# Performance work log

Measured on AMD Instinct MI355X. Metric: run time of the kernel, lower is better.

The kernel has to match this reference:

```python
import jax, jax.numpy as jnp
import numpy as np

D_MODEL = 512
NUM_HEADS = 8
D_HEAD = D_MODEL // NUM_HEADS
B, S = 2, 4096


def setup_inputs() -> dict:
    key = jax.random.key(0)
    ks = jax.random.split(key, 9)
    scale = 1.0 / np.sqrt(D_MODEL)
    x = jax.random.normal(ks[0], (B, S, D_MODEL), dtype=jnp.float32)
    Wq = jax.random.normal(ks[1], (D_MODEL, D_MODEL), dtype=jnp.float32) * scale
    Wk = jax.random.normal(ks[2], (D_MODEL, D_MODEL), dtype=jnp.float32) * scale
    Wv = jax.random.normal(ks[3], (D_MODEL, D_MODEL), dtype=jnp.float32) * scale
    Wo = jax.random.normal(ks[4], (D_MODEL, D_MODEL), dtype=jnp.float32) * scale
    bq = jnp.zeros((D_MODEL,), jnp.float32)
    bk = jnp.zeros((D_MODEL,), jnp.float32)
    bv = jnp.zeros((D_MODEL,), jnp.float32)
    bo = jnp.zeros((D_MODEL,), jnp.float32)
    return {"x": x, "Wq": Wq, "bq": bq, "Wk": Wk, "bk": bk,
            "Wv": Wv, "bv": bv, "Wo": Wo, "bo": bo}


def _split_heads(t):
    # [B, S, D] -> [B, H, S, d_head]
    b, s, _ = t.shape
    return t.reshape(b, s, NUM_HEADS, D_HEAD).transpose(0, 2, 1, 3)


def reference(x, Wq, bq, Wk, bk, Wv, bv, Wo, bo):
    q = _split_heads(x @ Wq + bq)  # [B,H,S,dh]
    k = _split_heads(x @ Wk + bk)
    v = _split_heads(x @ Wv + bv)
    scores = jnp.einsum("bhqd,bhkd->bhqk", q, k) / jnp.sqrt(
        jnp.asarray(D_HEAD, x.dtype))
    attn = jax.nn.softmax(scores, axis=-1)  # dropout is identity at inference
    out = jnp.einsum("bhqk,bhkd->bhqd", attn, v)  # [B,H,S,dh]
    out = out.transpose(0, 2, 1, 3).reshape(x.shape[0], x.shape[1], D_MODEL)
    return out @ Wo + bo
```

## Files before the change

### kernel.cpp

```cpp
#include <hip/hip_runtime.h>
#include <cstddef>

#define NB   2
#define SEQ  4096
#define DM   512
#define NH   8
#define DH   64
#define MTOT 8192
#define KSPLIT 4
#define KSEQ (SEQ / KSPLIT)

#define QSCALE 0.18033688011112042f

typedef __attribute__((ext_vector_type(8))) short short8;
typedef __attribute__((ext_vector_type(4))) float f32x4;

__device__ __forceinline__ ushort f2bf(float f) {
  unsigned u = __builtin_bit_cast(unsigned, f);
  u += 0x7FFFu + ((u >> 16) & 1u);
  return (ushort)(u >> 16);
}
__device__ __forceinline__ float bf2f(ushort b) {
  return __builtin_bit_cast(float, ((unsigned)b) << 16);
}
__device__ __forceinline__ unsigned cvt_pk_bf16(float lo, float hi) {
  unsigned r;
  asm("v_cvt_pk_bf16_f32 %0, %1, %2" : "=v"(r) : "v"(lo), "v"(hi));
  return r;
}
__device__ __forceinline__ float fexp2(float x) {
#if __has_builtin(__builtin_amdgcn_exp2f)
  return __builtin_amdgcn_exp2f(x);
#else
  float r;
  asm("v_exp_f32 %0, %1" : "=v"(r) : "v"(x));
  return r;
#endif
}

__global__ __launch_bounds__(256)
void prep_all_k(const float* __restrict__ x,
                const float* __restrict__ Wq, const float* __restrict__ Wk,
                const float* __restrict__ Wv, const float* __restrict__ Wo,
                ushort* __restrict__ xb,
                ushort* __restrict__ WTq, ushort* __restrict__ WTk,
                ushort* __restrict__ WTv, ushort* __restrict__ WTh,
                ushort* __restrict__ WTl) {
  __shared__ float t[32][33];
  int bid = blockIdx.x;
  if (bid < 2048) {
    const int i = (bid * 256 + threadIdx.x) * 8;
    float4 a = *(const float4*)(x + i);
    float4 b = *(const float4*)(x + i + 4);
    ushort h[8] = {f2bf(a.x), f2bf(a.y), f2bf(a.z), f2bf(a.w),
                   f2bf(b.x), f2bf(b.y), f2bf(b.z), f2bf(b.w)};
    *(uint4*)(xb + i) = *(const uint4*)h;
    return;
  }
  bid -= 2048;
  const int z = bid >> 8;
  const int rr = bid & 255;
  const float* W = (z == 0) ? Wq : (z == 1) ? Wk : (z == 2) ? Wv : Wo;
  ushort* WT = (z == 0) ? WTq : (z == 1) ? WTk : (z == 2) ? WTv : WTh;
  ushort* WTlo = (z == 3) ? WTl : nullptr;
  const int k0 = (rr & 15) * 32, n0 = (rr >> 4) * 32;
  const int tx = threadIdx.x & 31, ty = threadIdx.x >> 5;
#pragma unroll
  for (int i = 0; i < 32; i += 8)
    t[ty + i][tx] = W[(size_t)(k0 + ty + i) * DM + n0 + tx];
  __syncthreads();
#pragma unroll
  for (int i = 0; i < 32; i += 8) {
    float v = t[tx][ty + i];
    ushort h = f2bf(v);
    WT[(size_t)(n0 + ty + i) * DM + k0 + tx] = h;
    if (WTlo) WTlo[(size_t)(n0 + ty + i) * DM + k0 + tx] = f2bf(v - bf2f(h));
  }
}

__global__ __launch_bounds__(256)
void qkv_gemm_k(const ushort* __restrict__ xb,
                const ushort* __restrict__ WTq, const ushort* __restrict__ WTk,
                const ushort* __restrict__ WTv,
                const float* __restrict__ bq, const float* __restrict__ bk,
                const float* __restrict__ bv,
                ushort* __restrict__ Qb, ushort* __restrict__ Kb,
                ushort* __restrict__ Vb) {
  __shared__ ushort smem[17920];
  ushort (*As)[40] = (ushort(*)[40])smem;
  ushort (*Bs)[40] = (ushort(*)[40])(smem + 5120);

  const int z = blockIdx.z;
  const ushort* WT = (z == 0) ? WTq : (z == 1) ? WTk : WTv;
  const float* bias = (z == 0) ? bq : (z == 1) ? bk : bv;
  ushort* outp = (z == 0) ? Qb : (z == 1) ? Kb : Vb;
  const float oscale = (z == 0) ? QSCALE : 1.0f;

  const int tid = threadIdx.x;
  const int w = tid >> 6, l = tid & 63;
  const int g = l >> 4, l15 = l & 15;
  const int wm = w >> 1, wn = w & 1;
  const int m0 = blockIdx.x * 128;
  const int n0 = blockIdx.y * 128;

  const int ar = tid >> 1, ac = (tid & 1) * 16;
  const ushort* Ag = xb + (size_t)(m0 + ar) * DM + ac;
  const ushort* Bg = WT + (size_t)(n0 + ar) * DM + ac;

  uint4 ra0 = *(const uint4*)(Ag);
  uint4 ra1 = *(const uint4*)(Ag + 8);
  uint4 rb0 = *(const uint4*)(Bg);
  uint4 rb1 = *(const uint4*)(Bg + 8);

  float bfn[4];
#pragma unroll
  for (int fn = 0; fn < 4; ++fn)
    bfn[fn] = bias[n0 + wn * 64 + fn * 16 + l15];

  f32x4 acc[4][4];
#pragma unroll
  for (int fm = 0; fm < 4; ++fm)
#pragma unroll
    for (int fn = 0; fn < 4; ++fn) acc[fm][fn] = (f32x4){0.f, 0.f, 0.f, 0.f};

  for (int k0 = 0; k0 < DM; k0 += 32) {
    __syncthreads();
    *(uint4*)&As[ar][ac]     = ra0;
    *(uint4*)&As[ar][ac + 8] = ra1;
    *(uint4*)&Bs[ar][ac]     = rb0;
    *(uint4*)&Bs[ar][ac + 8] = rb1;
    __syncthreads();
    if (k0 + 32 < DM) {
      ra0 = *(const uint4*)(Ag + k0 + 32);
      ra1 = *(const uint4*)(Ag + k0 + 40);
      rb0 = *(const uint4*)(Bg + k0 + 32);
      rb1 = *(const uint4*)(Bg + k0 + 40);
    }
    short8 af[4], bf[4];
#pragma unroll
    for (int fm = 0; fm < 4; ++fm)
      af[fm] = *(const short8*)&As[wm * 64 + fm * 16 + l15][g * 8];
#pragma unroll
    for (int fn = 0; fn < 4; ++fn)
      bf[fn] = *(const short8*)&Bs[wn * 64 + fn * 16 + l15][g * 8];
#pragma unroll
    for (int fm = 0; fm < 4; ++fm)
#pragma unroll
      for (int fn = 0; fn < 4; ++fn)
        acc[fm][fn] = __builtin_amdgcn_mfma_f32_16x16x32_bf16(
            af[fm], bf[fn], acc[fm][fn], 0, 0, 0);
  }

  __syncthreads();
  ushort (*T)[140] = (ushort(*)[140])smem;
  const int b = m0 >> 12, s0 = m0 & (SEQ - 1);
  const int h0 = n0 >> 6;
  if (z != 2) {
#pragma unroll
    for (int fm = 0; fm < 4; ++fm)
#pragma unroll
      for (int fn = 0; fn < 4; ++fn)
#pragma unroll
        for (int r = 0; r < 4; ++r) {
          int ml = wm * 64 + fm * 16 + g * 4 + r;
          int nl = wn * 64 + fn * 16 + l15;
          T[ml][nl] = f2bf((acc[fm][fn][r] + bfn[fn]) * oscale);
        }
    __syncthreads();
#pragma unroll
    for (int it = 0; it < 8; ++it) {
      int ch = tid + 256 * it;
      int hl = ch >> 10;
      int sl = (ch >> 3) & 127;
      int c8 = (ch & 7) * 8;
      *(uint4*)(outp + ((size_t)(b * NH + h0 + hl) * SEQ + s0 + sl) * DH + c8) =
          *(const uint4*)&T[sl][hl * 64 + c8];
    }
  } else {
#pragma unroll
    for (int fm = 0; fm < 4; ++fm)
#pragma unroll
      for (int fn = 0; fn < 4; ++fn)
#pragma unroll
        for (int r = 0; r < 4; ++r) {
          int ml = wm * 64 + fm * 16 + g * 4 + r;
          int nl = wn * 64 + fn * 16 + l15;
          T[nl][ml] = f2bf(acc[fm][fn][r] + bfn[fn]);
        }
    __syncthreads();
#pragma unroll
    for (int it = 0; it < 8; ++it) {
      int ch = tid + 256 * it;
      int row = ch >> 4;
      int cc = (ch & 15) * 8;
      int n = n0 + row;
      int h = n >> 6, d = n & 63;
      *(uint4*)(outp + ((size_t)(b * NH + h) * DH + d) * SEQ + s0 + cc) =
          *(const uint4*)&T[row][cc];
    }
  }
}

__global__ __launch_bounds__(256)
void combine_k(const ushort* __restrict__ Po, const float* __restrict__ Dn,
               ushort* __restrict__ Ahb, ushort* __restrict__ Alb) {
  const size_t o = (size_t)(blockIdx.x * 256 + threadIdx.x) * 8;
  const int m = (int)(o >> 9);
  const int c = (int)(o & 511);
  const int b = m >> 12, s = m & (SEQ - 1);
  const int h = c >> 6, d = c & 63;
  const int bh = b * NH + h;
  const size_t i0 = ((size_t)bh * SEQ + s) * DH + d;
  const size_t zoff = (size_t)(NB * NH) * SEQ * DH;

  float den = 0.f;
  float v[8];
#pragma unroll
  for (int j = 0; j < 8; ++j) v[j] = 0.f;
#pragma unroll
  for (int z = 0; z < KSPLIT; ++z) {
    den += Dn[((size_t)z * (NB * NH) + bh) * SEQ + s];
    uint4 p = *(const uint4*)(Po + (size_t)z * zoff + i0);
    const unsigned* pu = (const unsigned*)&p;
#pragma unroll
    for (int j = 0; j < 4; ++j) {
      v[2 * j]     += __builtin_bit_cast(float, pu[j] << 16);
      v[2 * j + 1] += __builtin_bit_cast(float, pu[j] & 0xFFFF0000u);
    }
  }
  const float inv = __builtin_amdgcn_rcpf(den);
  ushort hh[8], ll[8];
#pragma unroll
  for (int j = 0; j < 8; ++j) {
    float a = v[j] * inv;
    ushort hb = f2bf(a);
    hh[j] = hb;
    ll[j] = f2bf(a - bf2f(hb));
  }
  *(uint4*)(Ahb + o) = *(const uint4*)hh;
  *(uint4*)(Alb + o) = *(const uint4*)ll;
}

__global__ __launch_bounds__(256)
void oproj_gemm_k(const ushort* __restrict__ Ahb, const ushort* __restrict__ Alb,
                  const ushort* __restrict__ WTh, const ushort* __restrict__ WTl,
                  const float* __restrict__ bo, float* __restrict__ out) {
  __shared__ ushort Ah[128][40];
  __shared__ ushort Al[128][40];
  __shared__ ushort Bh[128][40];
  __shared__ ushort Bl[128][40];

  const int tid = threadIdx.x;
  const int w = tid >> 6, l = tid & 63;
  const int g = l >> 4, l15 = l & 15;
  const int wm = w >> 1, wn = w & 1;
  const int m0 = blockIdx.x * 128;
  const int n0 = blockIdx.y * 128;

  const int ar = tid >> 1, ac = (tid & 1) * 16;

  const ushort* Ahg = Ahb + (size_t)(m0 + ar) * DM + ac;
  const ushort* Alg = Alb + (size_t)(m0 + ar) * DM + ac;
  const ushort* Bhg = WTh + (size_t)(n0 + ar) * DM + ac;
  const ushort* Blg = WTl + (size_t)(n0 + ar) * DM + ac;

  uint4 rah0 = *(const uint4*)(Ahg);
  uint4 rah1 = *(const uint4*)(Ahg + 8);
  uint4 ral0 = *(const uint4*)(Alg);
  uint4 ral1 = *(const uint4*)(Alg + 8);
  uint4 rbh0 = *(const uint4*)(Bhg);
  uint4 rbh1 = *(const uint4*)(Bhg + 8);
  uint4 rbl0 = *(const uint4*)(Blg);
  uint4 rbl1 = *(const uint4*)(Blg + 8);

  float bfn[4];
#pragma unroll
  for (int fn = 0; fn < 4; ++fn)
    bfn[fn] = bo[n0 + wn * 64 + fn * 16 + l15];

  f32x4 acc[4][4];
#pragma unroll
  for (int fm = 0; fm < 4; ++fm)
#pragma unroll
    for (int fn = 0; fn < 4; ++fn) acc[fm][fn] = (f32x4){0.f, 0.f, 0.f, 0.f};

  for (int k0 = 0; k0 < DM; k0 += 32) {
    __syncthreads();
    *(uint4*)&Ah[ar][ac]     = rah0;
    *(uint4*)&Ah[ar][ac + 8] = rah1;
    *(uint4*)&Al[ar][ac]     = ral0;
    *(uint4*)&Al[ar][ac + 8] = ral1;
    *(uint4*)&Bh[ar][ac]     = rbh0;
    *(uint4*)&Bh[ar][ac + 8] = rbh1;
    *(uint4*)&Bl[ar][ac]     = rbl0;
    *(uint4*)&Bl[ar][ac + 8] = rbl1;
    __syncthreads();
    if (k0 + 32 < DM) {
      rah0 = *(const uint4*)(Ahg + k0 + 32);
      rah1 = *(const uint4*)(Ahg + k0 + 40);
      ral0 = *(const uint4*)(Alg + k0 + 32);
      ral1 = *(const uint4*)(Alg + k0 + 40);
      rbh0 = *(const uint4*)(Bhg + k0 + 32);
      rbh1 = *(const uint4*)(Bhg + k0 + 40);
      rbl0 = *(const uint4*)(Blg + k0 + 32);
      rbl1 = *(const uint4*)(Blg + k0 + 40);
    }
    short8 ah[4], al[4], bh[4], bl[4];
#pragma unroll
    for (int fm = 0; fm < 4; ++fm) {
      ah[fm] = *(const short8*)&Ah[wm * 64 + fm * 16 + l15][g * 8];
      al[fm] = *(const short8*)&Al[wm * 64 + fm * 16 + l15][g * 8];
    }
#pragma unroll
    for (int fn = 0; fn < 4; ++fn) {
      bh[fn] = *(const short8*)&Bh[wn * 64 + fn * 16 + l15][g * 8];
      bl[fn] = *(const short8*)&Bl[wn * 64 + fn * 16 + l15][g * 8];
    }
#pragma unroll
    for (int fm = 0; fm < 4; ++fm)
#pragma unroll
      for (int fn = 0; fn < 4; ++fn) {
        f32x4 c = acc[fm][fn];
        c = __builtin_amdgcn_mfma_f32_16x16x32_bf16(ah[fm], bh[fn], c, 0, 0, 0);
        c = __builtin_amdgcn_mfma_f32_16x16x32_bf16(ah[fm], bl[fn], c, 0, 0, 0);
        c = __builtin_amdgcn_mfma_f32_16x16x32_bf16(al[fm], bh[fn], c, 0, 0, 0);
        acc[fm][fn] = c;
      }
  }

#pragma unroll
  for (int fm = 0; fm < 4; ++fm)
#pragma unroll
    for (int fn = 0; fn < 4; ++fn)
#pragma unroll
      for (int r = 0; r < 4; ++r) {
        int mm = m0 + wm * 64 + fm * 16 + g * 4 + r;
        int n = n0 + wn * 64 + fn * 16 + l15;
        out[(size_t)mm * DM + n] = acc[fm][fn][r] + bfn[fn];
      }
}

__global__ __launch_bounds__(256, 4)
void attn_mfma_k(const ushort* __restrict__ Q, const ushort* __restrict__ K,
                 const ushort* __restrict__ VT, ushort* __restrict__ Po,
                 float* __restrict__ Dn) {
  __shared__ ushort Ks[64][72];
  __shared__ unsigned Vt[64][36];

  const int tid = threadIdx.x;
  const int w   = tid >> 6;
  const int l   = tid & 63;
  const int g   = l >> 4;
  const int l15 = l & 15;
  const int bh  = blockIdx.y;
  const int z   = blockIdx.z;
  const int q0  = blockIdx.x * 128 + w * 32;
  const int tb  = z * KSEQ;

  short8 qb[2][2];
#pragma unroll
  for (int qh = 0; qh < 2; ++qh) {
    const ushort* Qrow = Q + ((size_t)bh * SEQ + q0 + qh * 16 + l15) * DH;
    qb[qh][0] = *(const short8*)(Qrow + g * 8);
    qb[qh][1] = *(const short8*)(Qrow + 32 + g * 8);
  }

  short8 vones;
#pragma unroll
  for (int i = 0; i < 8; ++i) vones[i] = (short)0x3F80;

  f32x4 acc[2][4];
  f32x4 accl[2];
#pragma unroll
  for (int qh = 0; qh < 2; ++qh) {
    accl[qh] = (f32x4){0.f, 0.f, 0.f, 0.f};
#pragma unroll
    for (int dt = 0; dt < 4; ++dt) acc[qh][dt] = (f32x4){0.f, 0.f, 0.f, 0.f};
  }

  const ushort* Kg = K + (size_t)bh * SEQ * DH;

  const int rho  = tid >> 2;
  const int kcol = (tid & 3) * 16;
  const int sig  = 32 * ((rho >> 5) & 1) + 8 * ((rho >> 2) & 3) +
                   4 * ((rho >> 4) & 1) + (rho & 3);
  const ushort* Kp = Kg + (size_t)(tb + sig) * DH + kcol;

  const int vrow = tid >> 2;
  const int vcb  = (tid & 3) * 8;
  const unsigned* Vrow =
      (const unsigned*)(VT + ((size_t)bh * DH + vrow) * SEQ) + tb / 2 + vcb;

  uint4 kr0 = *(const uint4*)(Kp);
  uint4 kr1 = *(const uint4*)(Kp + 8);
  uint4 vv0 = *(const uint4*)(Vrow);
  uint4 vv1 = *(const uint4*)(Vrow + 4);

  for (int t0 = 0; t0 < KSEQ; t0 += 64) {
    __syncthreads();
    *(uint4*)&Ks[rho][kcol]     = kr0;
    *(uint4*)&Ks[rho][kcol + 8] = kr1;
    *(uint4*)&Vt[vrow][vcb]     = vv0;
    *(uint4*)&Vt[vrow][vcb + 4] = vv1;
    if (t0 + 64 < KSEQ) {
      kr0 = *(const uint4*)(Kp + (size_t)(t0 + 64) * DH);
      kr1 = *(const uint4*)(Kp + (size_t)(t0 + 64) * DH + 8);
      vv0 = *(const uint4*)(Vrow + (t0 + 64) / 2);
      vv1 = *(const uint4*)(Vrow + (t0 + 64) / 2 + 4);
    }
    __syncthreads();

    f32x4 s[2][4];
    __builtin_amdgcn_s_setprio(1);
#pragma unroll
    for (int nf = 0; nf < 4; ++nf) {
      short8 ka0 = *(const short8*)&Ks[nf * 16 + l15][g * 8];
      short8 ka1 = *(const short8*)&Ks[nf * 16 + l15][32 + g * 8];
#pragma unroll
      for (int qh = 0; qh < 2; ++qh) {
        f32x4 c = (f32x4){0.f, 0.f, 0.f, 0.f};
        c = __builtin_amdgcn_mfma_f32_16x16x32_bf16(ka0, qb[qh][0], c, 0, 0, 0);
        c = __builtin_amdgcn_mfma_f32_16x16x32_bf16(ka1, qb[qh][1], c, 0, 0, 0);
        s[qh][nf] = c;
      }
    }
    __builtin_amdgcn_s_setprio(0);

    short8 pa[2][2];
#pragma unroll
    for (int qh = 0; qh < 2; ++qh) {
      float p[4][4];
#pragma unroll
      for (int nf = 0; nf < 4; ++nf)
#pragma unroll
        for (int r = 0; r < 4; ++r) p[nf][r] = fexp2(s[qh][nf][r]);
      uint4 u0, u1;
      u0.x = cvt_pk_bf16(p[0][0], p[0][1]);
      u0.y = cvt_pk_bf16(p[0][2], p[0][3]);
      u0.z = cvt_pk_bf16(p[1][0], p[1][1]);
      u0.w = cvt_pk_bf16(p[1][2], p[1][3]);
      u1.x = cvt_pk_bf16(p[2][0], p[2][1]);
      u1.y = cvt_pk_bf16(p[2][2], p[2][3]);
      u1.z = cvt_pk_bf16(p[3][0], p[3][1]);
      u1.w = cvt_pk_bf16(p[3][2], p[3][3]);
      pa[qh][0] = __builtin_bit_cast(short8, u0);
      pa[qh][1] = __builtin_bit_cast(short8, u1);
    }

    __builtin_amdgcn_s_setprio(1);
#pragma unroll
    for (int dt = 0; dt < 4; ++dt) {
      short8 vb0 = *(const short8*)&Vt[dt * 16 + l15][4 * g];
      short8 vb1 = *(const short8*)&Vt[dt * 16 + l15][16 + 4 * g];
#pragma unroll
      for (int qh = 0; qh < 2; ++qh) {
        acc[qh][dt] = __builtin_amdgcn_mfma_f32_16x16x32_bf16(pa[qh][0], vb0,
                                                              acc[qh][dt], 0, 0, 0);
        acc[qh][dt] = __builtin_amdgcn_mfma_f32_16x16x32_bf16(pa[qh][1], vb1,
                                                              acc[qh][dt], 0, 0, 0);
      }
    }
#pragma unroll
    for (int qh = 0; qh < 2; ++qh) {
      accl[qh] = __builtin_amdgcn_mfma_f32_16x16x32_bf16(pa[qh][0], vones,
                                                         accl[qh], 0, 0, 0);
      accl[qh] = __builtin_amdgcn_mfma_f32_16x16x32_bf16(pa[qh][1], vones,
                                                         accl[qh], 0, 0, 0);
    }
    __builtin_amdgcn_s_setprio(0);
  }

  const int zo = z * (NB * NH) + bh;
#pragma unroll
  for (int qh = 0; qh < 2; ++qh) {
#pragma unroll
    for (int dt = 0; dt < 4; ++dt)
#pragma unroll
      for (int r = 0; r < 4; ++r) {
        int srow = q0 + qh * 16 + g * 4 + r;
        Po[((size_t)zo * SEQ + srow) * DH + dt * 16 + l15] =
            f2bf(acc[qh][dt][r]);
      }
    if (l15 == 0)
#pragma unroll
      for (int r = 0; r < 4; ++r)
        Dn[(size_t)zo * SEQ + q0 + qh * 16 + g * 4 + r] = accl[qh][r];
  }
}

extern "C" void kernel_launch(void* const* d_in, const int* in_sizes, int n_in,
                              void* d_out, int out_size, void* d_ws, size_t ws_size,
                              hipStream_t stream) {
  const float* x  = (const float*)d_in[0];
  const float* Wq = (const float*)d_in[1];
  const float* bq = (const float*)d_in[2];
  const float* Wk = (const float*)d_in[3];
  const float* bk = (const float*)d_in[4];
  const float* Wv = (const float*)d_in[5];
  const float* bv = (const float*)d_in[6];
  const float* Wo = (const float*)d_in[7];
  const float* bo = (const float*)d_in[8];
  float* out = (float*)d_out;

  const size_t per = (size_t)NB * NH * SEQ * DH;
  const size_t wsz = (size_t)DM * DM;
  ushort* xb  = (ushort*)d_ws;
  ushort* WTq = xb + (size_t)MTOT * DM;
  ushort* WTk = WTq + wsz;
  ushort* WTv = WTk + wsz;
  ushort* WTh = WTv + wsz;
  ushort* WTl = WTh + wsz;
  ushort* Qb  = WTl + wsz;
  ushort* Kb  = Qb + per;
  ushort* Vb  = Kb + per;
  ushort* Po  = Vb + per;
  float*  Dn  = (float*)(Po + (size_t)KSPLIT * per);
  ushort* Ahb = xb;
  ushort* Alb = Qb;

  prep_all_k<<<3072, 256, 0, stream>>>(x, Wq, Wk, Wv, Wo, xb,
                                       WTq, WTk, WTv, WTh, WTl);
  qkv_gemm_k<<<dim3(MTOT / 128, DM / 128, 3), 256, 0, stream>>>(
      xb, WTq, WTk, WTv, bq, bk, bv, Qb, Kb, Vb);
  attn_mfma_k<<<dim3(SEQ / 128, NB * NH, KSPLIT), 256, 0, stream>>>(
      Qb, Kb, Vb, Po, Dn);
  combine_k<<<MTOT * DM / (256 * 8), 256, 0, stream>>>(Po, Dn, Ahb, Alb);
  oproj_gemm_k<<<dim3(MTOT / 128, DM / 128), 256, 0, stream>>>(
      Ahb, Alb, WTh, WTl, bo, out);
}
```

Before: 140.8 us.

## Drop split-bf16 output projection and shrink GEMM M-tiles to 64 rows

The output projection previously used hi/lo bf16 splitting of both activations and Wo, with three MFMAs per tile. It now uses a single bf16 pass, which removes the lo-part buffers, their writes in prep and combine, and two thirds of the oproj MFMA work. Separately, both the QKV and output-projection GEMMs move from 128x128 to 64x128 tiles, doubling the block count to improve occupancy and load balance. The cost is lower output accuracy from the plain bf16 matmul, and less data reuse per tile.

```diff
diff --git a/kernel.cpp b/kernel.cpp
--- a/kernel.cpp
+++ b/kernel.cpp
@@ -44,8 +44,7 @@
                 const float* __restrict__ Wv, const float* __restrict__ Wo,
                 ushort* __restrict__ xb,
                 ushort* __restrict__ WTq, ushort* __restrict__ WTk,
-                ushort* __restrict__ WTv, ushort* __restrict__ WTh,
-                ushort* __restrict__ WTl) {
+                ushort* __restrict__ WTv, ushort* __restrict__ WTh) {
   __shared__ float t[32][33];
   int bid = blockIdx.x;
   if (bid < 2048) {
@@ -62,7 +61,6 @@
   const int rr = bid & 255;
   const float* W = (z == 0) ? Wq : (z == 1) ? Wk : (z == 2) ? Wv : Wo;
   ushort* WT = (z == 0) ? WTq : (z == 1) ? WTk : (z == 2) ? WTv : WTh;
-  ushort* WTlo = (z == 3) ? WTl : nullptr;
   const int k0 = (rr & 15) * 32, n0 = (rr >> 4) * 32;
   const int tx = threadIdx.x & 31, ty = threadIdx.x >> 5;
 #pragma unroll
@@ -70,12 +68,8 @@
     t[ty + i][tx] = W[(size_t)(k0 + ty + i) * DM + n0 + tx];
   __syncthreads();
 #pragma unroll
-  for (int i = 0; i < 32; i += 8) {
-    float v = t[tx][ty + i];
-    ushort h = f2bf(v);
-    WT[(size_t)(n0 + ty + i) * DM + k0 + tx] = h;
-    if (WTlo) WTlo[(size_t)(n0 + ty + i) * DM + k0 + tx] = f2bf(v - bf2f(h));
-  }
+  for (int i = 0; i < 32; i += 8)
+    WT[(size_t)(n0 + ty + i) * DM + k0 + tx] = f2bf(t[tx][ty + i]);
 }
 
 __global__ __launch_bounds__(256)
@@ -86,9 +80,9 @@
                 const float* __restrict__ bv,
                 ushort* __restrict__ Qb, ushort* __restrict__ Kb,
                 ushort* __restrict__ Vb) {
-  __shared__ ushort smem[17920];
+  __shared__ ushort smem[9216];
   ushort (*As)[40] = (ushort(*)[40])smem;
-  ushort (*Bs)[40] = (ushort(*)[40])(smem + 5120);
+  ushort (*Bs)[40] = (ushort(*)[40])(smem + 2560);
 
   const int z = blockIdx.z;
   const ushort* WT = (z == 0) ? WTq : (z == 1) ? WTk : WTv;
@@ -100,15 +94,15 @@
   const int w = tid >> 6, l = tid & 63;
   const int g = l >> 4, l15 = l & 15;
   const int wm = w >> 1, wn = w & 1;
-  const int m0 = blockIdx.x * 128;
+  const int m0 = blockIdx.x * 64;
   const int n0 = blockIdx.y * 128;
 
-  const int ar = tid >> 1, ac = (tid & 1) * 16;
-  const ushort* Ag = xb + (size_t)(m0 + ar) * DM + ac;
-  const ushort* Bg = WT + (size_t)(n0 + ar) * DM + ac;
+  const int arA = tid >> 2, acA = (tid & 3) * 8;
+  const int arB = tid >> 1, acB = (tid & 1) * 16;
+  const ushort* Ag = xb + (size_t)(m0 + arA) * DM + acA;
+  const ushort* Bg = WT + (size_t)(n0 + arB) * DM + acB;
 
   uint4 ra0 = *(const uint4*)(Ag);
-  uint4 ra1 = *(const uint4*)(Ag + 8);
   uint4 rb0 = *(const uint4*)(Bg);
   uint4 rb1 = *(const uint4*)(Bg + 8);
 
@@ -117,34 +111,32 @@
   for (int fn = 0; fn < 4; ++fn)
     bfn[fn] = bias[n0 + wn * 64 + fn * 16 + l15];
 
-  f32x4 acc[4][4];
-#pragma unroll
-  for (int fm = 0; fm < 4; ++fm)
+  f32x4 acc[2][4];
+#pragma unroll
+  for (int fm = 0; fm < 2; ++fm)
 #pragma unroll
     for (int fn = 0; fn < 4; ++fn) acc[fm][fn] = (f32x4){0.f, 0.f, 0.f, 0.f};
 
   for (int k0 = 0; k0 < DM; k0 += 32) {
     __syncthreads();
-    *(uint4*)&As[ar][ac]     = ra0;
-    *(uint4*)&As[ar][ac + 8] = ra1;
-    *(uint4*)&Bs[ar][ac]     = rb0;
-    *(uint4*)&Bs[ar][ac + 8] = rb1;
+    *(uint4*)&As[arA][acA]     = ra0;
+    *(uint4*)&Bs[arB][acB]     = rb0;
+    *(uint4*)&Bs[arB][acB + 8] = rb1;
     __syncthreads();
     if (k0 + 32 < DM) {
       ra0 = *(const uint4*)(Ag + k0 + 32);
-      ra1 = *(const uint4*)(Ag + k0 + 40);
       rb0 = *(const uint4*)(Bg + k0 + 32);
       rb1 = *(const uint4*)(Bg + k0 + 40);
     }
-    short8 af[4], bf[4];
-#pragma unroll
-    for (int fm = 0; fm < 4; ++fm)
-      af[fm] = *(const short8*)&As[wm * 64 + fm * 16 + l15][g * 8];
+    short8 af[2], bf[4];
+#pragma unroll
+    for (int fm = 0; fm < 2; ++fm)
+      af[fm] = *(const short8*)&As[wm * 32 + fm * 16 + l15][g * 8];
 #pragma unroll
     for (int fn = 0; fn < 4; ++fn)
       bf[fn] = *(const short8*)&Bs[wn * 64 + fn * 16 + l15][g * 8];
 #pragma unroll
-    for (int fm = 0; fm < 4; ++fm)
+    for (int fm = 0; fm < 2; ++fm)
 #pragma unroll
       for (int fn = 0; fn < 4; ++fn)
         acc[fm][fn] = __builtin_amdgcn_mfma_f32_16x16x32_bf16(
@@ -152,47 +144,48 @@
   }
 
   __syncthreads();
-  ushort (*T)[140] = (ushort(*)[140])smem;
   const int b = m0 >> 12, s0 = m0 & (SEQ - 1);
   const int h0 = n0 >> 6;
   if (z != 2) {
-#pragma unroll
-    for (int fm = 0; fm < 4; ++fm)
+    ushort (*T)[136] = (ushort(*)[136])smem;
+#pragma unroll
+    for (int fm = 0; fm < 2; ++fm)
 #pragma unroll
       for (int fn = 0; fn < 4; ++fn)
 #pragma unroll
         for (int r = 0; r < 4; ++r) {
-          int ml = wm * 64 + fm * 16 + g * 4 + r;
+          int ml = wm * 32 + fm * 16 + g * 4 + r;
           int nl = wn * 64 + fn * 16 + l15;
           T[ml][nl] = f2bf((acc[fm][fn][r] + bfn[fn]) * oscale);
         }
     __syncthreads();
 #pragma unroll
-    for (int it = 0; it < 8; ++it) {
+    for (int it = 0; it < 4; ++it) {
       int ch = tid + 256 * it;
-      int hl = ch >> 10;
-      int sl = (ch >> 3) & 127;
+      int hl = ch >> 9;
+      int sl = (ch >> 3) & 63;
       int c8 = (ch & 7) * 8;
       *(uint4*)(outp + ((size_t)(b * NH + h0 + hl) * SEQ + s0 + sl) * DH + c8) =
           *(const uint4*)&T[sl][hl * 64 + c8];
     }
   } else {
-#pragma unroll
-    for (int fm = 0; fm < 4; ++fm)
+    ushort (*T)[72] = (ushort(*)[72])smem;
+#pragma unroll
+    for (int fm = 0; fm < 2; ++fm)
 #pragma unroll
       for (int fn = 0; fn < 4; ++fn)
 #pragma unroll
         for (int r = 0; r < 4; ++r) {
-          int ml = wm * 64 + fm * 16 + g * 4 + r;
+          int ml = wm * 32 + fm * 16 + g * 4 + r;
           int nl = wn * 64 + fn * 16 + l15;
           T[nl][ml] = f2bf(acc[fm][fn][r] + bfn[fn]);
         }
     __syncthreads();
 #pragma unroll
-    for (int it = 0; it < 8; ++it) {
+    for (int it = 0; it < 4; ++it) {
       int ch = tid + 256 * it;
-      int row = ch >> 4;
-      int cc = (ch & 15) * 8;
+      int row = ch >> 3;
+      int cc = (ch & 7) * 8;
       int n = n0 + row;
       int h = n >> 6, d = n & 63;
       *(uint4*)(outp + ((size_t)(b * NH + h) * DH + d) * SEQ + s0 + cc) =
@@ -203,7 +196,7 @@
 
 __global__ __launch_bounds__(256)
 void combine_k(const ushort* __restrict__ Po, const float* __restrict__ Dn,
-               ushort* __restrict__ Ahb, ushort* __restrict__ Alb) {
+               ushort* __restrict__ Ahb) {
   const size_t o = (size_t)(blockIdx.x * 256 + threadIdx.x) * 8;
   const int m = (int)(o >> 9);
   const int c = (int)(o & 511);
@@ -229,112 +222,78 @@
     }
   }
   const float inv = __builtin_amdgcn_rcpf(den);
-  ushort hh[8], ll[8];
-#pragma unroll
-  for (int j = 0; j < 8; ++j) {
-    float a = v[j] * inv;
-    ushort hb = f2bf(a);
-    hh[j] = hb;
-    ll[j] = f2bf(a - bf2f(hb));
-  }
+  ushort hh[8];
+#pragma unroll
+  for (int j = 0; j < 8; ++j) hh[j] = f2bf(v[j] * inv);
   *(uint4*)(Ahb + o) = *(const uint4*)hh;
-  *(uint4*)(Alb + o) = *(const uint4*)ll;
 }
 
 __global__ __launch_bounds__(256)
-void oproj_gemm_k(const ushort* __restrict__ Ahb, const ushort* __restrict__ Alb,
-                  const ushort* __restrict__ WTh, const ushort* __restrict__ WTl,
+void oproj_gemm_k(const ushort* __restrict__ Ahb, const ushort* __restrict__ WTh,
                   const float* __restrict__ bo, float* __restrict__ out) {
-  __shared__ ushort Ah[128][40];
-  __shared__ ushort Al[128][40];
-  __shared__ ushort Bh[128][40];
-  __shared__ ushort Bl[128][40];
+  __shared__ ushort As[64][40];
+  __shared__ ushort Bs[128][40];
 
   const int tid = threadIdx.x;
   const int w = tid >> 6, l = tid & 63;
   const int g = l >> 4, l15 = l & 15;
   const int wm = w >> 1, wn = w & 1;
-  const int m0 = blockIdx.x * 128;
+  const int m0 = blockIdx.x * 64;
   const int n0 = blockIdx.y * 128;
 
-  const int ar = tid >> 1, ac = (tid & 1) * 16;
-
-  const ushort* Ahg = Ahb + (size_t)(m0 + ar) * DM + ac;
-  const ushort* Alg = Alb + (size_t)(m0 + ar) * DM + ac;
-  const ushort* Bhg = WTh + (size_t)(n0 + ar) * DM + ac;
-  const ushort* Blg = WTl + (size_t)(n0 + ar) * DM + ac;
-
-  uint4 rah0 = *(const uint4*)(Ahg);
-  uint4 rah1 = *(const uint4*)(Ahg + 8);
-  uint4 ral0 = *(const uint4*)(Alg);
-  uint4 ral1 = *(const uint4*)(Alg + 8);
-  uint4 rbh0 = *(const uint4*)(Bhg);
-  uint4 rbh1 = *(const uint4*)(Bhg + 8);
-  uint4 rbl0 = *(const uint4*)(Blg);
-  uint4 rbl1 = *(const uint4*)(Blg + 8);
+  const int arA = tid >> 2, acA = (tid & 3) * 8;
+  const int arB = tid >> 1, acB = (tid & 1) * 16;
+  const ushort* Ag = Ahb + (size_t)(m0 + arA) * DM + acA;
+  const ushort* Bg = WTh + (size_t)(n0 + arB) * DM + acB;
+
+  uint4 ra0 = *(const uint4*)(Ag);
+  uint4 rb0 = *(const uint4*)(Bg);
+  uint4 rb1 = *(const uint4*)(Bg + 8);
 
   float bfn[4];
 #pragma unroll
   for (int fn = 0; fn < 4; ++fn)
     bfn[fn] = bo[n0 + wn * 64 + fn * 16 + l15];
 
-  f32x4 acc[4][4];
-#pragma unroll
-  for (int fm = 0; fm < 4; ++fm)
+  f32x4 acc[2][4];
+#pragma unroll
+  for (int fm = 0; fm < 2; ++fm)
 #pragma unroll
     for (int fn = 0; fn < 4; ++fn) acc[fm][fn] = (f32x4){0.f, 0.f, 0.f, 0.f};
 
   for (int k0 = 0; k0 < DM; k0 += 32) {
     __syncthreads();
-    *(uint4*)&Ah[ar][ac]     = rah0;
-    *(uint4*)&Ah[ar][ac + 8] = rah1;
-    *(uint4*)&Al[ar][ac]     = ral0;
-    *(uint4*)&Al[ar][ac + 8] = ral1;
-    *(uint4*)&Bh[ar][ac]     = rbh0;
-    *(uint4*)&Bh[ar][ac + 8] = rbh1;
-    *(uint4*)&Bl[ar][ac]     = rbl0;
-    *(uint4*)&Bl[ar][ac + 8] = rbl1;
+    *(uint4*)&As[arA][acA]     = ra0;
+    *(uint4*)&Bs[arB][acB]     = rb0;
+    *(uint4*)&Bs[arB][acB + 8] = rb1;
     __syncthreads();
     if (k0 + 32 < DM) {
-      rah0 = *(const uint4*)(Ahg + k0 + 32);
-      rah1 = *(const uint4*)(Ahg + k0 + 40);
-      ral0 = *(const uint4*)(Alg + k0 + 32);
-      ral1 = *(const uint4*)(Alg + k0 + 40);
-      rbh0 = *(const uint4*)(Bhg + k0 + 32);
-      rbh1 = *(const uint4*)(Bhg + k0 + 40);
-      rbl0 = *(const uint4*)(Blg + k0 + 32);
-      rbl1 = *(const uint4*)(Blg + k0 + 40);
-    }
-    short8 ah[4], al[4], bh[4], bl[4];
-#pragma unroll
-    for (int fm = 0; fm < 4; ++fm) {
-      ah[fm] = *(const short8*)&Ah[wm * 64 + fm * 16 + l15][g * 8];
-      al[fm] = *(const short8*)&Al[wm * 64 + fm * 16 + l15][g * 8];
-    }
-#pragma unroll
-    for (int fn = 0; fn < 4; ++fn) {
-      bh[fn] = *(const short8*)&Bh[wn * 64 + fn * 16 + l15][g * 8];
-      bl[fn] = *(const short8*)&Bl[wn * 64 + fn * 16 + l15][g * 8];
-    }
-#pragma unroll
-    for (int fm = 0; fm < 4; ++fm)
-#pragma unroll
-      for (int fn = 0; fn < 4; ++fn) {
-        f32x4 c = acc[fm][fn];
-        c = __builtin_amdgcn_mfma_f32_16x16x32_bf16(ah[fm], bh[fn], c, 0, 0, 0);
-        c = __builtin_amdgcn_mfma_f32_16x16x32_bf16(ah[fm], bl[fn], c, 0, 0, 0);
-        c = __builtin_amdgcn_mfma_f32_16x16x32_bf16(al[fm], bh[fn], c, 0, 0, 0);
-        acc[fm][fn] = c;
-      }
-  }
-
-#pragma unroll
-  for (int fm = 0; fm < 4; ++fm)
+      ra0 = *(const uint4*)(Ag + k0 + 32);
+      rb0 = *(const uint4*)(Bg + k0 + 32);
+      rb1 = *(const uint4*)(Bg + k0 + 40);
+    }
+    short8 af[2], bf[4];
+#pragma unroll
+    for (int fm = 0; fm < 2; ++fm)
+      af[fm] = *(const short8*)&As[wm * 32 + fm * 16 + l15][g * 8];
 #pragma unroll
     for (int fn = 0; fn < 4; ++fn)
+      bf[fn] = *(const short8*)&Bs[wn * 64 + fn * 16 + l15][g * 8];
+#pragma unroll
+    for (int fm = 0; fm < 2; ++fm)
+#pragma unroll
+      for (int fn = 0; fn < 4; ++fn)
+        acc[fm][fn] = __builtin_amdgcn_mfma_f32_16x16x32_bf16(
+            af[fm], bf[fn], acc[fm][fn], 0, 0, 0);
+  }
+
+#pragma unroll
+  for (int fm = 0; fm < 2; ++fm)
+#pragma unroll
+    for (int fn = 0; fn < 4; ++fn)
 #pragma unroll
       for (int r = 0; r < 4; ++r) {
-        int mm = m0 + wm * 64 + fm * 16 + g * 4 + r;
+        int mm = m0 + wm * 32 + fm * 16 + g * 4 + r;
         int n = n0 + wn * 64 + fn * 16 + l15;
         out[(size_t)mm * DM + n] = acc[fm][fn][r] + bfn[fn];
       }
@@ -509,22 +468,20 @@
   ushort* WTk = WTq + wsz;
   ushort* WTv = WTk + wsz;
   ushort* WTh = WTv + wsz;
-  ushort* WTl = WTh + wsz;
-  ushort* Qb  = WTl + wsz;
+  ushort* Qb  = WTh + wsz;
   ushort* Kb  = Qb + per;
   ushort* Vb  = Kb + per;
   ushort* Po  = Vb + per;
   float*  Dn  = (float*)(Po + (size_t)KSPLIT * per);
   ushort* Ahb = xb;
-  ushort* Alb = Qb;
 
   prep_all_k<<<3072, 256, 0, stream>>>(x, Wq, Wk, Wv, Wo, xb,
-                                       WTq, WTk, WTv, WTh, WTl);
-  qkv_gemm_k<<<dim3(MTOT / 128, DM / 128, 3), 256, 0, stream>>>(
+                                       WTq, WTk, WTv, WTh);
+  qkv_gemm_k<<<dim3(MTOT / 64, DM / 128, 3), 256, 0, stream>>>(
       xb, WTq, WTk, WTv, bq, bk, bv, Qb, Kb, Vb);
   attn_mfma_k<<<dim3(SEQ / 128, NB * NH, KSPLIT), 256, 0, stream>>>(
       Qb, Kb, Vb, Po, Dn);
-  combine_k<<<MTOT * DM / (256 * 8), 256, 0, stream>>>(Po, Dn, Ahb, Alb);
-  oproj_gemm_k<<<dim3(MTOT / 128, DM / 128), 256, 0, stream>>>(
-      Ahb, Alb, WTh, WTl, bo, out);
-}
+  combine_k<<<MTOT * DM / (256 * 8), 256, 0, stream>>>(Po, Dn, Ahb);
+  oproj_gemm_k<<<dim3(MTOT / 64, DM / 128), 256, 0, stream>>>(
+      Ahb, WTh, bo, out);
+}
```

Result: faster. 131.0 us (-7.0%).
